# Performance work log

Hardware: AMD Instinct MI355X
Metric: run time of the kernel (lower is better)

Reference implementation:

```python
import jax, jax.numpy as jnp
import numpy as np

B, S, D = 2, 2048, 1024
H, HD = 16, 64


def setup_inputs() -> dict:
    key = jax.random.key(0)
    ks = jax.random.split(key, 6)
    hidden_states = jax.random.normal(ks[0], (B, S, D), dtype=jnp.float32)
    c_attn_w = jax.random.normal(ks[1], (D, 3 * D), dtype=jnp.float32) * 0.02
    c_attn_b = jnp.zeros((3 * D,), dtype=jnp.float32)
    c_proj_w = jax.random.normal(ks[2], (D, D), dtype=jnp.float32) * 0.02
    c_proj_b = jnp.zeros((D,), dtype=jnp.float32)
    basis = jax.random.normal(ks[3], (H, HD, HD), dtype=jnp.float32) * 0.1
    projectors = jnp.einsum('hdr,her->hde', basis, basis)  # basis @ basis.T per head
    return {
        'hidden_states': hidden_states,
        'c_attn_w': c_attn_w,
        'c_attn_b': c_attn_b,
        'c_proj_w': c_proj_w,
        'c_proj_b': c_proj_b,
        'projectors': projectors,
    }


def reference(hidden_states, c_attn_w, c_attn_b, c_proj_w, c_proj_b, projectors):
    # GPT2 Conv1D: out = x @ W + b
    qkv = hidden_states @ c_attn_w + c_attn_b  # [B,S,3D]
    q, k, v = jnp.split(qkv, 3, axis=-1)
    # split heads -> [B,H,S,HD]
    def split_heads(t):
        return t.reshape(B, S, H, HD).transpose(0, 2, 1, 3)
    q, k, v = split_heads(q), split_heads(k), split_heads(v)
    scores = jnp.einsum('bhqd,bhkd->bhqk', q, k) / jnp.sqrt(jnp.float32(HD))
    causal = jnp.tril(jnp.ones((S, S), dtype=bool))
    scores = jnp.where(causal, scores, jnp.finfo(scores.dtype).min)
    probs = jax.nn.softmax(scores, axis=-1)
    attn = jnp.einsum('bhqk,bhkd->bhqd', probs, v)  # [B,H,S,HD]
    # per-head basis projector applied to attention output
    attn = jnp.einsum('bhsd,hde->bhse', attn, projectors)
    # merge heads -> [B,S,D]
    attn = attn.transpose(0, 2, 1, 3).reshape(B, S, D)
    out = attn @ c_proj_w + c_proj_b
    return out
```

## Files before the change

### kernel.cpp

```cpp
#include <hip/hip_runtime.h>

typedef __attribute__((ext_vector_type(8))) short bhalf8;
typedef __attribute__((ext_vector_type(4))) float f32x4;
typedef __attribute__((ext_vector_type(8))) unsigned short u16x8;
typedef __attribute__((ext_vector_type(4))) unsigned short u16x4;

#define BDIM 2
#define SDIM 2048
#define DDIM 1024
#define HDIM 16
#define HDHD 64

__device__ __forceinline__ unsigned short f2bf(float f) {
  unsigned u = __builtin_bit_cast(unsigned, f);
  u += 0x7fffu + ((u >> 16) & 1u);
  return (unsigned short)(u >> 16);
}

__global__ __launch_bounds__(256) void cvt_hidden(const float* __restrict__ x,
                                                  unsigned short* __restrict__ y) {
  size_t i = ((size_t)blockIdx.x * 256 + threadIdx.x) * 4;
  f32x4 v = *(const f32x4*)(x + i);
  u16x4 o;
  o[0] = f2bf(v[0]); o[1] = f2bf(v[1]); o[2] = f2bf(v[2]); o[3] = f2bf(v[3]);
  *(u16x4*)(y + i) = o;
}

__global__ __launch_bounds__(256) void transpose_cvt(const float* __restrict__ W,
                                                     unsigned short* __restrict__ Wt,
                                                     int R, int C) {
  __shared__ float tl[32][33];
  int rt = blockIdx.x * 32, ct = blockIdx.y * 32;
  int r8 = threadIdx.x >> 5, c = threadIdx.x & 31;
#pragma unroll
  for (int i = 0; i < 4; i++)
    tl[r8 + i * 8][c] = W[(size_t)(rt + r8 + i * 8) * C + ct + c];
  __syncthreads();
#pragma unroll
  for (int i = 0; i < 4; i++)
    Wt[(size_t)(ct + r8 + i * 8) * R + rt + c] = f2bf(tl[c][r8 + i * 8]);
}

__global__ __launch_bounds__(256) void make_wproj(const float* __restrict__ proj,
                                                  const float* __restrict__ wproj,
                                                  unsigned short* __restrict__ WT) {
  int h = blockIdx.x, ot = blockIdx.y * 64;
  __shared__ float Pl[64][65];
  __shared__ float Wl[64][65];
  int t = threadIdx.x;
#pragma unroll
  for (int i = 0; i < 16; i++) {
    int idx = t + 256 * i;
    int a = idx >> 6, bc = idx & 63;
    Pl[a][bc] = proj[(size_t)h * 4096 + idx];
    Wl[a][bc] = wproj[(size_t)(h * 64 + a) * 1024 + ot + bc];
  }
  __syncthreads();
  int d = t & 63, ob = t >> 6;
#pragma unroll
  for (int i = 0; i < 16; i++) {
    int o = ob + i * 4;
    float acc = 0.f;
#pragma unroll
    for (int e = 0; e < 64; e++) acc += Pl[d][e] * Wl[e][o];
    WT[(size_t)(ot + o) * 1024 + h * 64 + d] = f2bf(acc);
  }
}

template <int EPI>
__global__ __launch_bounds__(256) void gemm_bt(
    const unsigned short* __restrict__ A, const unsigned short* __restrict__ Bt,
    const float* __restrict__ bias, float* __restrict__ Cf,
    unsigned short* __restrict__ q, unsigned short* __restrict__ k,
    unsigned short* __restrict__ v, int M, int N, int K) {
  __shared__ unsigned short As[128][72];
  __shared__ unsigned short Bs[128][72];
  const int tid = threadIdx.x;
  const int m0 = blockIdx.y * 128, n0 = blockIdx.x * 128;
  f32x4 acc[4][4];
#pragma unroll
  for (int m = 0; m < 4; m++)
#pragma unroll
    for (int n = 0; n < 4; n++) acc[m][n] = f32x4{0.f, 0.f, 0.f, 0.f};
  const int w = tid >> 6, lane = tid & 63;
  const int wr = (w >> 1) * 64, wc = (w & 1) * 64;
  const int lrow = lane & 15, lk = (lane >> 4) * 8;

  for (int kt = 0; kt < K; kt += 64) {
    __syncthreads();
#pragma unroll
    for (int i = 0; i < 4; i++) {
      int cch = tid + 256 * i;
      int r = cch >> 3, c8 = cch & 7;
      *(u16x8*)(&As[r][c8 * 8]) = *(const u16x8*)(A + (size_t)(m0 + r) * K + kt + c8 * 8);
      *(u16x8*)(&Bs[r][c8 * 8]) = *(const u16x8*)(Bt + (size_t)(n0 + r) * K + kt + c8 * 8);
    }
    __syncthreads();
#pragma unroll
    for (int kk = 0; kk < 2; kk++) {
      bhalf8 af[4], bfr[4];
#pragma unroll
      for (int m = 0; m < 4; m++) af[m] = *(const bhalf8*)(&As[wr + m * 16 + lrow][kk * 32 + lk]);
#pragma unroll
      for (int n = 0; n < 4; n++) bfr[n] = *(const bhalf8*)(&Bs[wc + n * 16 + lrow][kk * 32 + lk]);
#pragma unroll
      for (int m = 0; m < 4; m++)
#pragma unroll
        for (int n = 0; n < 4; n++)
          acc[m][n] = __builtin_amdgcn_mfma_f32_16x16x32_bf16(af[m], bfr[n], acc[m][n], 0, 0, 0);
    }
  }
  const int g = lane >> 4, il = lane & 15;
#pragma unroll
  for (int m = 0; m < 4; m++) {
    int rowb = wr + m * 16 + 4 * g;
#pragma unroll
    for (int n = 0; n < 4; n++) {
      int col = n0 + wc + n * 16 + il;
      float bs = bias[col];
#pragma unroll
      for (int r = 0; r < 4; r++) {
        int row = m0 + rowb + r;
        float val = acc[m][n][r] + bs;
        if (EPI == 0) {
          int which = col >> 10, hh = (col >> 6) & 15, hd = col & 63;
          int b = row >> 11, s = row & 2047;
          size_t idx = ((size_t)(b * 16 + hh) * SDIM + s) * HDHD + hd;
          unsigned short bv = f2bf(which == 0 ? val * 0.125f : val);
          if (which == 0) q[idx] = bv;
          else if (which == 1) k[idx] = bv;
          else v[idx] = bv;
        } else {
          Cf[(size_t)row * N + col] = val;
        }
      }
    }
  }
}

__global__ __launch_bounds__(256, 4) void attn_kernel(const unsigned short* __restrict__ Q,
                                                      const unsigned short* __restrict__ Kb,
                                                      const unsigned short* __restrict__ Vb,
                                                      unsigned short* __restrict__ Om) {
  __shared__ unsigned short Ks[64][72];
  __shared__ unsigned short Vt[64][72];
  __shared__ unsigned short Ps[4][16][72];
  const int bh = blockIdx.x;
  const int qt = 31 - blockIdx.y;
  const int tid = threadIdx.x;
  const int w = tid >> 6, lane = tid & 63;
  const int g = lane >> 4, il = lane & 15;
  const int qbase = qt * 64 + w * 16;
  const size_t bhS = (size_t)bh * SDIM;

  bhalf8 qf0, qf1;
  {
    const unsigned short* qp = Q + (bhS + qbase + il) * HDHD + g * 8;
    qf0 = *(const bhalf8*)(qp);
    qf1 = *(const bhalf8*)(qp + 32);
  }
  f32x4 oacc[4];
#pragma unroll
  for (int i = 0; i < 4; i++) oacc[i] = f32x4{0.f, 0.f, 0.f, 0.f};
  float mrun[4], lrun[4];
#pragma unroll
  for (int r = 0; r < 4; r++) { mrun[r] = -1e30f; lrun[r] = 0.f; }

  const int srow = tid >> 2;
  const int schk = (tid & 3) * 16;
  const int nt = qt + 1;

  for (int kt = 0; kt < nt; kt++) {
    const size_t kbase = (bhS + (size_t)kt * 64) * HDHD;
    __syncthreads();
    {
      const unsigned short* src = Kb + kbase + srow * HDHD + schk;
      *(u16x8*)(&Ks[srow][schk]) = *(const u16x8*)(src);
      *(u16x8*)(&Ks[srow][schk + 8]) = *(const u16x8*)(src + 8);
    }
    {
      const unsigned short* vsrc = Vb + kbase + (size_t)(w * 16) * HDHD + lane;
      u16x8 va, vb2;
#pragma unroll
      for (int i = 0; i < 8; i++) va[i] = vsrc[i * HDHD];
#pragma unroll
      for (int i = 0; i < 8; i++) vb2[i] = vsrc[(8 + i) * HDHD];
      *(u16x8*)(&Vt[lane][w * 16]) = va;
      *(u16x8*)(&Vt[lane][w * 16 + 8]) = vb2;
    }
    __syncthreads();
    f32x4 s[4];
#pragma unroll
    for (int c = 0; c < 4; c++) s[c] = f32x4{0.f, 0.f, 0.f, 0.f};
#pragma unroll
    for (int c = 0; c < 4; c++) {
      bhalf8 k0 = *(const bhalf8*)(&Ks[c * 16 + il][g * 8]);
      bhalf8 k1 = *(const bhalf8*)(&Ks[c * 16 + il][32 + g * 8]);
      s[c] = __builtin_amdgcn_mfma_f32_16x16x32_bf16(qf0, k0, s[c], 0, 0, 0);
      s[c] = __builtin_amdgcn_mfma_f32_16x16x32_bf16(qf1, k1, s[c], 0, 0, 0);
    }
    const bool diag = (kt == qt);
    const int kc0 = kt * 64 + il;
#pragma unroll
    for (int r = 0; r < 4; r++) {
      float v0 = s[0][r], v1 = s[1][r], v2 = s[2][r], v3 = s[3][r];
      if (diag) {
        int qr = qbase + 4 * g + r;
        if (kc0 > qr) v0 = -1e30f;
        if (kc0 + 16 > qr) v1 = -1e30f;
        if (kc0 + 32 > qr) v2 = -1e30f;
        if (kc0 + 48 > qr) v3 = -1e30f;
      }
      float mx = fmaxf(fmaxf(v0, v1), fmaxf(v2, v3));
      mx = fmaxf(mx, __shfl_xor(mx, 1));
      mx = fmaxf(mx, __shfl_xor(mx, 2));
      mx = fmaxf(mx, __shfl_xor(mx, 4));
      mx = fmaxf(mx, __shfl_xor(mx, 8));
      float mn = fmaxf(mrun[r], mx);
      float sc = __expf(mrun[r] - mn);
      mrun[r] = mn;
      float p0 = __expf(v0 - mn), p1 = __expf(v1 - mn);
      float p2 = __expf(v2 - mn), p3 = __expf(v3 - mn);
      float rs = p0 + p1 + p2 + p3;
      rs += __shfl_xor(rs, 1);
      rs += __shfl_xor(rs, 2);
      rs += __shfl_xor(rs, 4);
      rs += __shfl_xor(rs, 8);
      lrun[r] = lrun[r] * sc + rs;
      int pr = 4 * g + r;
      Ps[w][pr][il] = f2bf(p0);
      Ps[w][pr][16 + il] = f2bf(p1);
      Ps[w][pr][32 + il] = f2bf(p2);
      Ps[w][pr][48 + il] = f2bf(p3);
#pragma unroll
      for (int df = 0; df < 4; df++) oacc[df][r] *= sc;
    }
#pragma unroll
    for (int kk = 0; kk < 2; kk++) {
      bhalf8 pf = *(const bhalf8*)(&Ps[w][il][kk * 32 + g * 8]);
#pragma unroll
      for (int df = 0; df < 4; df++) {
        bhalf8 vf = *(const bhalf8*)(&Vt[df * 16 + il][kk * 32 + g * 8]);
        oacc[df] = __builtin_amdgcn_mfma_f32_16x16x32_bf16(pf, vf, oacc[df], 0, 0, 0);
      }
    }
  }
  const int b = bh >> 4, h = bh & 15;
#pragma unroll
  for (int r = 0; r < 4; r++) {
    int srow2 = qbase + 4 * g + r;
    float inv = 1.f / lrun[r];
#pragma unroll
    for (int df = 0; df < 4; df++) {
      Om[((size_t)b * SDIM + srow2) * DDIM + h * HDHD + df * 16 + il] =
          f2bf(oacc[df][r] * inv);
    }
  }
}

extern "C" void kernel_launch(void* const* d_in, const int* in_sizes, int n_in,
                              void* d_out, int out_size, void* d_ws, size_t ws_size,
                              hipStream_t stream) {
  const float* hidden = (const float*)d_in[0];
  const float* attn_w = (const float*)d_in[1];
  const float* attn_b = (const float*)d_in[2];
  const float* proj_w = (const float*)d_in[3];
  const float* proj_b = (const float*)d_in[4];
  const float* projectors = (const float*)d_in[5];
  float* out = (float*)d_out;
  char* ws = (char*)d_ws;
  (void)in_sizes; (void)n_in; (void)out_size; (void)ws_size;

  unsigned short* hseq   = (unsigned short*)(ws);
  unsigned short* wqkvT  = (unsigned short*)(ws + 8388608);
  unsigned short* qb     = (unsigned short*)(ws + 14680064);
  unsigned short* kb     = (unsigned short*)(ws + 23068672);
  unsigned short* vb     = (unsigned short*)(ws + 31457280);
  unsigned short* attnM  = (unsigned short*)(ws + 39845888);
  unsigned short* wprojT = (unsigned short*)(ws + 48234496);

  cvt_hidden<<<dim3(4096), dim3(256), 0, stream>>>(hidden, hseq);
  transpose_cvt<<<dim3(32, 96), dim3(256), 0, stream>>>(attn_w, wqkvT, 1024, 3072);
  make_wproj<<<dim3(16, 16), dim3(256), 0, stream>>>(projectors, proj_w, wprojT);
  gemm_bt<0><<<dim3(24, 32), dim3(256), 0, stream>>>(hseq, wqkvT, attn_b, nullptr,
                                                     qb, kb, vb, 4096, 3072, 1024);
  attn_kernel<<<dim3(32, 32), dim3(256), 0, stream>>>(qb, kb, vb, attnM);
  gemm_bt<1><<<dim3(8, 32), dim3(256), 0, stream>>>(attnM, wprojT, proj_b, out,
                                                    nullptr, nullptr, nullptr, 4096, 1024, 1024);
}
```

Baseline: 176.9 us.

## Double attention query tile to 128 rows and use exp2 softmax

```diff
diff --git a/kernel.cpp b/kernel.cpp
--- a/kernel.cpp
+++ b/kernel.cpp
@@ -126,7 +126,7 @@
           int which = col >> 10, hh = (col >> 6) & 15, hd = col & 63;
           int b = row >> 11, s = row & 2047;
           size_t idx = ((size_t)(b * 16 + hh) * SDIM + s) * HDHD + hd;
-          unsigned short bv = f2bf(which == 0 ? val * 0.125f : val);
+          unsigned short bv = f2bf(which == 0 ? val * 0.1803368801f : val);
           if (which == 0) q[idx] = bv;
           else if (which == 1) k[idx] = bv;
           else v[idx] = bv;
@@ -144,31 +144,36 @@
                                                       unsigned short* __restrict__ Om) {
   __shared__ unsigned short Ks[64][72];
   __shared__ unsigned short Vt[64][72];
-  __shared__ unsigned short Ps[4][16][72];
+  __shared__ unsigned short Ps[4][32][72];
   const int bh = blockIdx.x;
-  const int qt = 31 - blockIdx.y;
+  const int qt = 15 - blockIdx.y;
   const int tid = threadIdx.x;
   const int w = tid >> 6, lane = tid & 63;
   const int g = lane >> 4, il = lane & 15;
-  const int qbase = qt * 64 + w * 16;
+  const int qbase = qt * 128 + w * 32;
   const size_t bhS = (size_t)bh * SDIM;
 
-  bhalf8 qf0, qf1;
-  {
-    const unsigned short* qp = Q + (bhS + qbase + il) * HDHD + g * 8;
-    qf0 = *(const bhalf8*)(qp);
-    qf1 = *(const bhalf8*)(qp + 32);
-  }
-  f32x4 oacc[4];
-#pragma unroll
-  for (int i = 0; i < 4; i++) oacc[i] = f32x4{0.f, 0.f, 0.f, 0.f};
-  float mrun[4], lrun[4];
-#pragma unroll
-  for (int r = 0; r < 4; r++) { mrun[r] = -1e30f; lrun[r] = 0.f; }
+  bhalf8 qf[2][2];
+#pragma unroll
+  for (int f = 0; f < 2; f++) {
+    const unsigned short* qp = Q + (bhS + qbase + f * 16 + il) * HDHD + g * 8;
+    qf[f][0] = *(const bhalf8*)(qp);
+    qf[f][1] = *(const bhalf8*)(qp + 32);
+  }
+  f32x4 oacc[2][4];
+#pragma unroll
+  for (int f = 0; f < 2; f++)
+#pragma unroll
+    for (int i = 0; i < 4; i++) oacc[f][i] = f32x4{0.f, 0.f, 0.f, 0.f};
+  float mrun[2][4], lrun[2][4];
+#pragma unroll
+  for (int f = 0; f < 2; f++)
+#pragma unroll
+    for (int r = 0; r < 4; r++) { mrun[f][r] = -1e30f; lrun[f][r] = 0.f; }
 
   const int srow = tid >> 2;
   const int schk = (tid & 3) * 16;
-  const int nt = qt + 1;
+  const int nt = 2 * qt + 2;
 
   for (int kt = 0; kt < nt; kt++) {
     const size_t kbase = (bhS + (size_t)kt * 64) * HDHD;
@@ -189,71 +194,84 @@
       *(u16x8*)(&Vt[lane][w * 16 + 8]) = vb2;
     }
     __syncthreads();
-    f32x4 s[4];
-#pragma unroll
-    for (int c = 0; c < 4; c++) s[c] = f32x4{0.f, 0.f, 0.f, 0.f};
+    f32x4 s[2][4];
+#pragma unroll
+    for (int f = 0; f < 2; f++)
+#pragma unroll
+      for (int c = 0; c < 4; c++) s[f][c] = f32x4{0.f, 0.f, 0.f, 0.f};
 #pragma unroll
     for (int c = 0; c < 4; c++) {
       bhalf8 k0 = *(const bhalf8*)(&Ks[c * 16 + il][g * 8]);
       bhalf8 k1 = *(const bhalf8*)(&Ks[c * 16 + il][32 + g * 8]);
-      s[c] = __builtin_amdgcn_mfma_f32_16x16x32_bf16(qf0, k0, s[c], 0, 0, 0);
-      s[c] = __builtin_amdgcn_mfma_f32_16x16x32_bf16(qf1, k1, s[c], 0, 0, 0);
-    }
-    const bool diag = (kt == qt);
+#pragma unroll
+      for (int f = 0; f < 2; f++) {
+        s[f][c] = __builtin_amdgcn_mfma_f32_16x16x32_bf16(qf[f][0], k0, s[f][c], 0, 0, 0);
+        s[f][c] = __builtin_amdgcn_mfma_f32_16x16x32_bf16(qf[f][1], k1, s[f][c], 0, 0, 0);
+      }
+    }
+    const bool diag = (kt >= 2 * qt);
     const int kc0 = kt * 64 + il;
 #pragma unroll
-    for (int r = 0; r < 4; r++) {
-      float v0 = s[0][r], v1 = s[1][r], v2 = s[2][r], v3 = s[3][r];
-      if (diag) {
-        int qr = qbase + 4 * g + r;
-        if (kc0 > qr) v0 = -1e30f;
-        if (kc0 + 16 > qr) v1 = -1e30f;
-        if (kc0 + 32 > qr) v2 = -1e30f;
-        if (kc0 + 48 > qr) v3 = -1e30f;
-      }
-      float mx = fmaxf(fmaxf(v0, v1), fmaxf(v2, v3));
-      mx = fmaxf(mx, __shfl_xor(mx, 1));
-      mx = fmaxf(mx, __shfl_xor(mx, 2));
-      mx = fmaxf(mx, __shfl_xor(mx, 4));
-      mx = fmaxf(mx, __shfl_xor(mx, 8));
-      float mn = fmaxf(mrun[r], mx);
-      float sc = __expf(mrun[r] - mn);
-      mrun[r] = mn;
-      float p0 = __expf(v0 - mn), p1 = __expf(v1 - mn);
-      float p2 = __expf(v2 - mn), p3 = __expf(v3 - mn);
-      float rs = p0 + p1 + p2 + p3;
-      rs += __shfl_xor(rs, 1);
-      rs += __shfl_xor(rs, 2);
-      rs += __shfl_xor(rs, 4);
-      rs += __shfl_xor(rs, 8);
-      lrun[r] = lrun[r] * sc + rs;
-      int pr = 4 * g + r;
-      Ps[w][pr][il] = f2bf(p0);
-      Ps[w][pr][16 + il] = f2bf(p1);
-      Ps[w][pr][32 + il] = f2bf(p2);
-      Ps[w][pr][48 + il] = f2bf(p3);
-#pragma unroll
-      for (int df = 0; df < 4; df++) oacc[df][r] *= sc;
+    for (int f = 0; f < 2; f++) {
+#pragma unroll
+      for (int r = 0; r < 4; r++) {
+        float v0 = s[f][0][r], v1 = s[f][1][r], v2 = s[f][2][r], v3 = s[f][3][r];
+        if (diag) {
+          int qr = qbase + f * 16 + 4 * g + r;
+          if (kc0 > qr) v0 = -1e30f;
+          if (kc0 + 16 > qr) v1 = -1e30f;
+          if (kc0 + 32 > qr) v2 = -1e30f;
+          if (kc0 + 48 > qr) v3 = -1e30f;
+        }
+        float mx = fmaxf(fmaxf(v0, v1), fmaxf(v2, v3));
+        mx = fmaxf(mx, __shfl_xor(mx, 1));
+        mx = fmaxf(mx, __shfl_xor(mx, 2));
+        mx = fmaxf(mx, __shfl_xor(mx, 4));
+        mx = fmaxf(mx, __shfl_xor(mx, 8));
+        float mn = fmaxf(mrun[f][r], mx);
+        float sc = exp2f(mrun[f][r] - mn);
+        mrun[f][r] = mn;
+        float p0 = exp2f(v0 - mn), p1 = exp2f(v1 - mn);
+        float p2 = exp2f(v2 - mn), p3 = exp2f(v3 - mn);
+        float rs = p0 + p1 + p2 + p3;
+        rs += __shfl_xor(rs, 1);
+        rs += __shfl_xor(rs, 2);
+        rs += __shfl_xor(rs, 4);
+        rs += __shfl_xor(rs, 8);
+        lrun[f][r] = lrun[f][r] * sc + rs;
+        int pr = f * 16 + 4 * g + r;
+        Ps[w][pr][il] = f2bf(p0);
+        Ps[w][pr][16 + il] = f2bf(p1);
+        Ps[w][pr][32 + il] = f2bf(p2);
+        Ps[w][pr][48 + il] = f2bf(p3);
+#pragma unroll
+        for (int df = 0; df < 4; df++) oacc[f][df][r] *= sc;
+      }
     }
 #pragma unroll
     for (int kk = 0; kk < 2; kk++) {
-      bhalf8 pf = *(const bhalf8*)(&Ps[w][il][kk * 32 + g * 8]);
+      bhalf8 pf0 = *(const bhalf8*)(&Ps[w][il][kk * 32 + g * 8]);
+      bhalf8 pf1 = *(const bhalf8*)(&Ps[w][16 + il][kk * 32 + g * 8]);
 #pragma unroll
       for (int df = 0; df < 4; df++) {
         bhalf8 vf = *(const bhalf8*)(&Vt[df * 16 + il][kk * 32 + g * 8]);
-        oacc[df] = __builtin_amdgcn_mfma_f32_16x16x32_bf16(pf, vf, oacc[df], 0, 0, 0);
+        oacc[0][df] = __builtin_amdgcn_mfma_f32_16x16x32_bf16(pf0, vf, oacc[0][df], 0, 0, 0);
+        oacc[1][df] = __builtin_amdgcn_mfma_f32_16x16x32_bf16(pf1, vf, oacc[1][df], 0, 0, 0);
       }
     }
   }
   const int b = bh >> 4, h = bh & 15;
 #pragma unroll
-  for (int r = 0; r < 4; r++) {
-    int srow2 = qbase + 4 * g + r;
-    float inv = 1.f / lrun[r];
-#pragma unroll
-    for (int df = 0; df < 4; df++) {
-      Om[((size_t)b * SDIM + srow2) * DDIM + h * HDHD + df * 16 + il] =
-          f2bf(oacc[df][r] * inv);
+  for (int f = 0; f < 2; f++) {
+#pragma unroll
+    for (int r = 0; r < 4; r++) {
+      int srow2 = qbase + f * 16 + 4 * g + r;
+      float inv = 1.f / lrun[f][r];
+#pragma unroll
+      for (int df = 0; df < 4; df++) {
+        Om[((size_t)b * SDIM + srow2) * DDIM + h * HDHD + df * 16 + il] =
+            f2bf(oacc[f][df][r] * inv);
+      }
     }
   }
 }
@@ -284,7 +302,7 @@
   make_wproj<<<dim3(16, 16), dim3(256), 0, stream>>>(projectors, proj_w, wprojT);
   gemm_bt<0><<<dim3(24, 32), dim3(256), 0, stream>>>(hseq, wqkvT, attn_b, nullptr,
                                                      qb, kb, vb, 4096, 3072, 1024);
-  attn_kernel<<<dim3(32, 32), dim3(256), 0, stream>>>(qb, kb, vb, attnM);
+  attn_kernel<<<dim3(32, 16), dim3(256), 0, stream>>>(qb, kb, vb, attnM);
   gemm_bt<1><<<dim3(8, 32), dim3(256), 0, stream>>>(attnM, wprojT, proj_b, out,
                                                     nullptr, nullptr, nullptr, 4096, 1024, 1024);
 }
```

After: 249.3 us. 40.9% more time.

## Split causal attention along KV into segments with a separate merge kernel

Applied to the files above, without the earlier changes.

```diff
diff --git a/kernel.cpp b/kernel.cpp
--- a/kernel.cpp
+++ b/kernel.cpp
@@ -15,6 +15,9 @@
   unsigned u = __builtin_bit_cast(unsigned, f);
   u += 0x7fffu + ((u >> 16) & 1u);
   return (unsigned short)(u >> 16);
+}
+__device__ __forceinline__ float bf2f(unsigned short u) {
+  return __builtin_bit_cast(float, (unsigned)u << 16);
 }
 
 __global__ __launch_bounds__(256) void cvt_hidden(const float* __restrict__ x,
@@ -126,7 +129,7 @@
           int which = col >> 10, hh = (col >> 6) & 15, hd = col & 63;
           int b = row >> 11, s = row & 2047;
           size_t idx = ((size_t)(b * 16 + hh) * SDIM + s) * HDHD + hd;
-          unsigned short bv = f2bf(which == 0 ? val * 0.125f : val);
+          unsigned short bv = f2bf(which == 0 ? val * 0.1803368801f : val);
           if (which == 0) q[idx] = bv;
           else if (which == 1) k[idx] = bv;
           else v[idx] = bv;
@@ -138,15 +141,23 @@
   }
 }
 
-__global__ __launch_bounds__(256, 4) void attn_kernel(const unsigned short* __restrict__ Q,
-                                                      const unsigned short* __restrict__ Kb,
-                                                      const unsigned short* __restrict__ Vb,
-                                                      unsigned short* __restrict__ Om) {
+__global__ __launch_bounds__(256, 4) void attn_partial(const unsigned short* __restrict__ Q,
+                                                       const unsigned short* __restrict__ Kb,
+                                                       const unsigned short* __restrict__ Vb,
+                                                       unsigned short* __restrict__ PO,
+                                                       float2* __restrict__ ML) {
+  const int bh = blockIdx.x;
+  const int qt = 31 - blockIdx.y;
+  const int seg = blockIdx.z;
+  const int a = qt >> 3, bq = qt & 7;
+  const int nseg = a + 1;
+  if (seg >= nseg) return;
+  const int k0 = seg * 8;
+  const int k1 = min(k0 + 8, qt + 1);
+
   __shared__ unsigned short Ks[64][72];
   __shared__ unsigned short Vt[64][72];
   __shared__ unsigned short Ps[4][16][72];
-  const int bh = blockIdx.x;
-  const int qt = 31 - blockIdx.y;
   const int tid = threadIdx.x;
   const int w = tid >> 6, lane = tid & 63;
   const int g = lane >> 4, il = lane & 15;
@@ -168,9 +179,8 @@
 
   const int srow = tid >> 2;
   const int schk = (tid & 3) * 16;
-  const int nt = qt + 1;
-
-  for (int kt = 0; kt < nt; kt++) {
+
+  for (int kt = k0; kt < k1; kt++) {
     const size_t kbase = (bhS + (size_t)kt * 64) * HDHD;
     __syncthreads();
     {
@@ -194,10 +204,10 @@
     for (int c = 0; c < 4; c++) s[c] = f32x4{0.f, 0.f, 0.f, 0.f};
 #pragma unroll
     for (int c = 0; c < 4; c++) {
-      bhalf8 k0 = *(const bhalf8*)(&Ks[c * 16 + il][g * 8]);
-      bhalf8 k1 = *(const bhalf8*)(&Ks[c * 16 + il][32 + g * 8]);
-      s[c] = __builtin_amdgcn_mfma_f32_16x16x32_bf16(qf0, k0, s[c], 0, 0, 0);
-      s[c] = __builtin_amdgcn_mfma_f32_16x16x32_bf16(qf1, k1, s[c], 0, 0, 0);
+      bhalf8 kf0 = *(const bhalf8*)(&Ks[c * 16 + il][g * 8]);
+      bhalf8 kf1 = *(const bhalf8*)(&Ks[c * 16 + il][32 + g * 8]);
+      s[c] = __builtin_amdgcn_mfma_f32_16x16x32_bf16(qf0, kf0, s[c], 0, 0, 0);
+      s[c] = __builtin_amdgcn_mfma_f32_16x16x32_bf16(qf1, kf1, s[c], 0, 0, 0);
     }
     const bool diag = (kt == qt);
     const int kc0 = kt * 64 + il;
@@ -217,10 +227,10 @@
       mx = fmaxf(mx, __shfl_xor(mx, 4));
       mx = fmaxf(mx, __shfl_xor(mx, 8));
       float mn = fmaxf(mrun[r], mx);
-      float sc = __expf(mrun[r] - mn);
+      float sc = exp2f(mrun[r] - mn);
       mrun[r] = mn;
-      float p0 = __expf(v0 - mn), p1 = __expf(v1 - mn);
-      float p2 = __expf(v2 - mn), p3 = __expf(v3 - mn);
+      float p0 = exp2f(v0 - mn), p1 = exp2f(v1 - mn);
+      float p2 = exp2f(v2 - mn), p3 = exp2f(v3 - mn);
       float rs = p0 + p1 + p2 + p3;
       rs += __shfl_xor(rs, 1);
       rs += __shfl_xor(rs, 2);
@@ -245,6 +255,165 @@
       }
     }
   }
+  const int pidx = bh * 80 + 4 * a * (a + 1) + bq * (a + 1) + seg;
+#pragma unroll
+  for (int r = 0; r < 4; r++) {
+    int rl = w * 16 + 4 * g + r;
+    float inv = 1.f / lrun[r];
+#pragma unroll
+    for (int df = 0; df < 4; df++)
+      PO[(size_t)pidx * 4096 + rl * 64 + df * 16 + il] = f2bf(oacc[df][r] * inv);
+    if (il == 0) ML[(size_t)pidx * 64 + rl] = make_float2(mrun[r], lrun[r]);
+  }
+}
+
+__global__ __launch_bounds__(256) void attn_reduce(const unsigned short* __restrict__ PO,
+                                                   const float2* __restrict__ ML,
+                                                   unsigned short* __restrict__ Om) {
+  const int bh = blockIdx.x, qt = blockIdx.y;
+  const int a = qt >> 3, bq = qt & 7;
+  const int nseg = a + 1;
+  const int base = bh * 80 + 4 * a * (a + 1) + bq * (a + 1);
+  const int t = threadIdx.x;
+  const int r = t >> 2, dc = (t & 3) * 16;
+  float2 mls[4];
+  float M = -1e30f;
+#pragma unroll
+  for (int s = 0; s < 4; s++) {
+    if (s < nseg) { mls[s] = ML[(size_t)(base + s) * 64 + r]; M = fmaxf(M, mls[s].x); }
+  }
+  float L = 0.f;
+  float O[16];
+#pragma unroll
+  for (int j = 0; j < 16; j++) O[j] = 0.f;
+#pragma unroll
+  for (int s = 0; s < 4; s++) {
+    if (s < nseg) {
+      float wgt = mls[s].y * exp2f(mls[s].x - M);
+      L += wgt;
+      const unsigned short* p = PO + (size_t)(base + s) * 4096 + r * 64 + dc;
+      u16x8 p0 = *(const u16x8*)p, p1 = *(const u16x8*)(p + 8);
+#pragma unroll
+      for (int j = 0; j < 8; j++) O[j] += wgt * bf2f(p0[j]);
+#pragma unroll
+      for (int j = 0; j < 8; j++) O[8 + j] += wgt * bf2f(p1[j]);
+    }
+  }
+  float inv = 1.f / L;
+  const int b = bh >> 4, h = bh & 15;
+  size_t orow = ((size_t)b * SDIM + qt * 64 + r) * DDIM + h * HDHD + dc;
+  u16x8 o0, o1;
+#pragma unroll
+  for (int j = 0; j < 8; j++) o0[j] = f2bf(O[j] * inv);
+#pragma unroll
+  for (int j = 0; j < 8; j++) o1[j] = f2bf(O[8 + j] * inv);
+  *(u16x8*)(Om + orow) = o0;
+  *(u16x8*)(Om + orow + 8) = o1;
+}
+
+__global__ __launch_bounds__(256, 4) void attn_direct(const unsigned short* __restrict__ Q,
+                                                      const unsigned short* __restrict__ Kb,
+                                                      const unsigned short* __restrict__ Vb,
+                                                      unsigned short* __restrict__ Om) {
+  __shared__ unsigned short Ks[64][72];
+  __shared__ unsigned short Vt[64][72];
+  __shared__ unsigned short Ps[4][16][72];
+  const int bh = blockIdx.x;
+  const int qt = 31 - blockIdx.y;
+  const int tid = threadIdx.x;
+  const int w = tid >> 6, lane = tid & 63;
+  const int g = lane >> 4, il = lane & 15;
+  const int qbase = qt * 64 + w * 16;
+  const size_t bhS = (size_t)bh * SDIM;
+  bhalf8 qf0, qf1;
+  {
+    const unsigned short* qp = Q + (bhS + qbase + il) * HDHD + g * 8;
+    qf0 = *(const bhalf8*)(qp);
+    qf1 = *(const bhalf8*)(qp + 32);
+  }
+  f32x4 oacc[4];
+#pragma unroll
+  for (int i = 0; i < 4; i++) oacc[i] = f32x4{0.f, 0.f, 0.f, 0.f};
+  float mrun[4], lrun[4];
+#pragma unroll
+  for (int r = 0; r < 4; r++) { mrun[r] = -1e30f; lrun[r] = 0.f; }
+  const int srow = tid >> 2, schk = (tid & 3) * 16;
+  const int nt = qt + 1;
+  for (int kt = 0; kt < nt; kt++) {
+    const size_t kbase = (bhS + (size_t)kt * 64) * HDHD;
+    __syncthreads();
+    {
+      const unsigned short* src = Kb + kbase + srow * HDHD + schk;
+      *(u16x8*)(&Ks[srow][schk]) = *(const u16x8*)(src);
+      *(u16x8*)(&Ks[srow][schk + 8]) = *(const u16x8*)(src + 8);
+    }
+    {
+      const unsigned short* vsrc = Vb + kbase + (size_t)(w * 16) * HDHD + lane;
+      u16x8 va, vb2;
+#pragma unroll
+      for (int i = 0; i < 8; i++) va[i] = vsrc[i * HDHD];
+#pragma unroll
+      for (int i = 0; i < 8; i++) vb2[i] = vsrc[(8 + i) * HDHD];
+      *(u16x8*)(&Vt[lane][w * 16]) = va;
+      *(u16x8*)(&Vt[lane][w * 16 + 8]) = vb2;
+    }
+    __syncthreads();
+    f32x4 s[4];
+#pragma unroll
+    for (int c = 0; c < 4; c++) s[c] = f32x4{0.f, 0.f, 0.f, 0.f};
+#pragma unroll
+    for (int c = 0; c < 4; c++) {
+      bhalf8 kf0 = *(const bhalf8*)(&Ks[c * 16 + il][g * 8]);
+      bhalf8 kf1 = *(const bhalf8*)(&Ks[c * 16 + il][32 + g * 8]);
+      s[c] = __builtin_amdgcn_mfma_f32_16x16x32_bf16(qf0, kf0, s[c], 0, 0, 0);
+      s[c] = __builtin_amdgcn_mfma_f32_16x16x32_bf16(qf1, kf1, s[c], 0, 0, 0);
+    }
+    const bool diag = (kt == qt);
+    const int kc0 = kt * 64 + il;
+#pragma unroll
+    for (int r = 0; r < 4; r++) {
+      float v0 = s[0][r], v1 = s[1][r], v2 = s[2][r], v3 = s[3][r];
+      if (diag) {
+        int qr = qbase + 4 * g + r;
+        if (kc0 > qr) v0 = -1e30f;
+        if (kc0 + 16 > qr) v1 = -1e30f;
+        if (kc0 + 32 > qr) v2 = -1e30f;
+        if (kc0 + 48 > qr) v3 = -1e30f;
+      }
+      float mx = fmaxf(fmaxf(v0, v1), fmaxf(v2, v3));
+      mx = fmaxf(mx, __shfl_xor(mx, 1));
+      mx = fmaxf(mx, __shfl_xor(mx, 2));
+      mx = fmaxf(mx, __shfl_xor(mx, 4));
+      mx = fmaxf(mx, __shfl_xor(mx, 8));
+      float mn = fmaxf(mrun[r], mx);
+      float sc = exp2f(mrun[r] - mn);
+      mrun[r] = mn;
+      float p0 = exp2f(v0 - mn), p1 = exp2f(v1 - mn);
+      float p2 = exp2f(v2 - mn), p3 = exp2f(v3 - mn);
+      float rs = p0 + p1 + p2 + p3;
+      rs += __shfl_xor(rs, 1);
+      rs += __shfl_xor(rs, 2);
+      rs += __shfl_xor(rs, 4);
+      rs += __shfl_xor(rs, 8);
+      lrun[r] = lrun[r] * sc + rs;
+      int pr = 4 * g + r;
+      Ps[w][pr][il] = f2bf(p0);
+      Ps[w][pr][16 + il] = f2bf(p1);
+      Ps[w][pr][32 + il] = f2bf(p2);
+      Ps[w][pr][48 + il] = f2bf(p3);
+#pragma unroll
+      for (int df = 0; df < 4; df++) oacc[df][r] *= sc;
+    }
+#pragma unroll
+    for (int kk = 0; kk < 2; kk++) {
+      bhalf8 pf = *(const bhalf8*)(&Ps[w][il][kk * 32 + g * 8]);
+#pragma unroll
+      for (int df = 0; df < 4; df++) {
+        bhalf8 vf = *(const bhalf8*)(&Vt[df * 16 + il][kk * 32 + g * 8]);
+        oacc[df] = __builtin_amdgcn_mfma_f32_16x16x32_bf16(pf, vf, oacc[df], 0, 0, 0);
+      }
+    }
+  }
   const int b = bh >> 4, h = bh & 15;
 #pragma unroll
   for (int r = 0; r < 4; r++) {
@@ -269,7 +438,7 @@
   const float* projectors = (const float*)d_in[5];
   float* out = (float*)d_out;
   char* ws = (char*)d_ws;
-  (void)in_sizes; (void)n_in; (void)out_size; (void)ws_size;
+  (void)in_sizes; (void)n_in; (void)out_size;
 
   unsigned short* hseq   = (unsigned short*)(ws);
   unsigned short* wqkvT  = (unsigned short*)(ws + 8388608);
@@ -278,13 +447,21 @@
   unsigned short* vb     = (unsigned short*)(ws + 31457280);
   unsigned short* attnM  = (unsigned short*)(ws + 39845888);
   unsigned short* wprojT = (unsigned short*)(ws + 48234496);
+  unsigned short* PO     = (unsigned short*)(ws + 50331648);
+  float2*         ML2    = (float2*)(ws + 71303168);
+  const size_t ws_needed = 71303168 + 1310720;
 
   cvt_hidden<<<dim3(4096), dim3(256), 0, stream>>>(hidden, hseq);
   transpose_cvt<<<dim3(32, 96), dim3(256), 0, stream>>>(attn_w, wqkvT, 1024, 3072);
   make_wproj<<<dim3(16, 16), dim3(256), 0, stream>>>(projectors, proj_w, wprojT);
   gemm_bt<0><<<dim3(24, 32), dim3(256), 0, stream>>>(hseq, wqkvT, attn_b, nullptr,
                                                      qb, kb, vb, 4096, 3072, 1024);
-  attn_kernel<<<dim3(32, 32), dim3(256), 0, stream>>>(qb, kb, vb, attnM);
+  if (ws_size >= ws_needed) {
+    attn_partial<<<dim3(32, 32, 4), dim3(256), 0, stream>>>(qb, kb, vb, PO, ML2);
+    attn_reduce<<<dim3(32, 32), dim3(256), 0, stream>>>(PO, ML2, attnM);
+  } else {
+    attn_direct<<<dim3(32, 32), dim3(256), 0, stream>>>(qb, kb, vb, attnM);
+  }
   gemm_bt<1><<<dim3(8, 32), dim3(256), 0, stream>>>(attnM, wprojT, proj_b, out,
                                                     nullptr, nullptr, nullptr, 4096, 1024, 1024);
 }
```

Result: slower. 186.4 us (+5.3%).
